# Kernel optimization log

Hardware: AMD Instinct MI355X
Metric: run time of the kernel (lower is better)

Reference implementation:

```python
import jax, jax.numpy as jnp
import numpy as np

B, S, H, L, NH, V = 8, 512, 768, 12, 12, 21128
DH = H // NH
FF = 4 * H
PAD_ID, SEP_ID = 0, 102
EPS = 1e-12


def _ln(x, g, b):
    mu = jnp.mean(x, axis=-1, keepdims=True)
    var = jnp.mean(jnp.square(x - mu), axis=-1, keepdims=True)
    return (x - mu) * jax.lax.rsqrt(var + EPS) * g + b


def setup_inputs() -> dict:
    key = jax.random.key(0)
    ks = jax.random.split(key, 24)
    # token ids with a per-sample [SEP] boundary and trailing padding
    ids = jax.random.randint(ks[0], (B, S), 1, V)
    qpos = jax.random.randint(ks[1], (B,), 16, 64)
    seqlen = jax.random.randint(ks[2], (B,), 384, S + 1)
    pos = jnp.arange(S)
    ids = jnp.where(pos[None, :] == qpos[:, None], SEP_ID, ids)
    ids = jnp.where(pos[None, :] < seqlen[:, None], ids, PAD_ID)

    w = lambda k, shape: (jax.random.normal(k, shape, dtype=jnp.float32) * 0.02)
    return {
        "input_ids": ids,
        "word_emb": w(ks[3], (V, H)),
        "pos_emb": w(ks[4], (S, H)),
        "type_emb": w(ks[5], (2, H)),
        "emb_ln_g": jnp.ones((H,), jnp.float32),
        "emb_ln_b": jnp.zeros((H,), jnp.float32),
        "attn_w": w(ks[6], (L, 4, H, H)),     # q,k,v,o projections
        "attn_b": w(ks[7], (L, 4, H)),
        "ln1_g": jnp.ones((L, H), jnp.float32),
        "ln1_b": jnp.zeros((L, H), jnp.float32),
        "ffn_w1": w(ks[8], (L, H, FF)),
        "ffn_b1": w(ks[9], (L, FF)),
        "ffn_w2": w(ks[10], (L, FF, H)),
        "ffn_b2": w(ks[11], (L, H)),
        "ln2_g": jnp.ones((L, H), jnp.float32),
        "ln2_b": jnp.zeros((L, H), jnp.float32),
        "cls_w": w(ks[12], (H, V)),
        "cls_b": jnp.zeros((V,), jnp.float32),
    }


def _qa_causal_bias(input_ids):
    # Faithful to make_qa_causal_mask: pad mask * (bidirectional over question,
    # causal over answer), boundary = first [SEP] position + 1 per sample.
    pad = input_ids != PAD_ID                                  # [B,S]
    qlen = jnp.argmax(input_ids == SEP_ID, axis=1) + 1          # [B]
    i = jnp.arange(S)[:, None]
    j = jnp.arange(S)[None, :]
    in_answer = (i[None] >= qlen[:, None, None]) & (j[None] >= qlen[:, None, None])
    causal_ok = jnp.where(in_answer, j <= i, True)              # [B,S,S]
    mask = pad[:, :, None] & pad[:, None, :] & causal_ok
    return jnp.where(mask, 0.0, -1e9).astype(jnp.float32)       # additive bias


def reference(input_ids, word_emb, pos_emb, type_emb, emb_ln_g, emb_ln_b,
              attn_w, attn_b, ln1_g, ln1_b, ffn_w1, ffn_b1, ffn_w2, ffn_b2,
              ln2_g, ln2_b, cls_w, cls_b):
    bias = _qa_causal_bias(input_ids)[:, None]                  # [B,1,S,S]
    h = word_emb[input_ids] + pos_emb[None, :S] + type_emb[0]
    h = _ln(h, emb_ln_g, emb_ln_b)
    scale = 1.0 / jnp.sqrt(jnp.float32(DH))
    for l in range(L):
        wq, wk, wv, wo = attn_w[l]
        bq, bk, bv, bo = attn_b[l]
        q = (h @ wq + bq).reshape(B, S, NH, DH)
        k = (h @ wk + bk).reshape(B, S, NH, DH)
        v = (h @ wv + bv).reshape(B, S, NH, DH)
        scores = jnp.einsum('bqhd,bkhd->bhqk', q, k) * scale + bias
        probs = jax.nn.softmax(scores, axis=-1)
        ctx = jnp.einsum('bhqk,bkhd->bqhd', probs, v).reshape(B, S, H)
        h = _ln(h + ctx @ wo + bo, ln1_g[l], ln1_b[l])
        ff = jax.nn.gelu(h @ ffn_w1[l] + ffn_b1[l], approximate=False) @ ffn_w2[l] + ffn_b2[l]
        h = _ln(h + ff, ln2_g[l], ln2_b[l])
    return h @ cls_w + cls_b                                    # [B,S,V] logits
```

## Files before the change

kernel.cpp:

```cpp
#include <hip/hip_runtime.h>
#include <hip/hip_bf16.h>
#include <stdint.h>

#define BB   8
#define SS   512
#define HH   768
#define LL   12
#define NHH  12
#define DHH  64
#define FFF  3072
#define VV   21128
#define PAD_ID 0
#define SEP_ID 102
#define BS   (BB*SS)
#define BSH  ((size_t)BS*HH)
#define BSFF ((size_t)BS*FFF)
#define QKVN (3*HH)

using bf16 = __hip_bfloat16;
typedef __attribute__((ext_vector_type(8))) short short8;
typedef __attribute__((ext_vector_type(4))) float f32x4;

__device__ __forceinline__ f32x4 Z4() { f32x4 z = {0.f, 0.f, 0.f, 0.f}; return z; }

__device__ __forceinline__ void gload16(void* lds, const void* g) {
    __builtin_amdgcn_global_load_lds(
        (const __attribute__((address_space(1))) uint32_t*)g,
        (__attribute__((address_space(3))) uint32_t*)(uint32_t)(uintptr_t)lds,
        16, 0, 0);
}

__device__ __forceinline__ void wait_vm0_barrier() {
    asm volatile("s_waitcnt vmcnt(0)" ::: "memory");
    __builtin_amdgcn_sched_barrier(0);
    __builtin_amdgcn_s_barrier();
    __builtin_amdgcn_sched_barrier(0);
}

__device__ __forceinline__ void wait_vm0_lgkm0_barrier() {
    asm volatile("s_waitcnt vmcnt(0) lgkmcnt(0)" ::: "memory");
    __builtin_amdgcn_sched_barrier(0);
    __builtin_amdgcn_s_barrier();
    __builtin_amdgcn_sched_barrier(0);
}

__global__ void __launch_bounds__(256) qlen_kernel(const int* __restrict__ ids,
                                                   int* __restrict__ qlen) {
    int b = blockIdx.x, tid = threadIdx.x;
    __shared__ int red[256];
    int best = 1 << 30;
    for (int j = tid; j < SS; j += 256)
        if (ids[b * SS + j] == SEP_ID) best = min(best, j);
    red[tid] = best; __syncthreads();
    for (int off = 128; off > 0; off >>= 1) {
        if (tid < off) red[tid] = min(red[tid], red[tid + off]);
        __syncthreads();
    }
    if (tid == 0) qlen[b] = (red[0] == (1 << 30) ? 0 : red[0]) + 1;
}

__device__ __forceinline__ float block_reduce_sum(float v, float* red, int tid) {
    red[tid] = v; __syncthreads();
    for (int off = 128; off > 0; off >>= 1) {
        if (tid < off) red[tid] += red[tid + off];
        __syncthreads();
    }
    float r = red[0]; __syncthreads();
    return r;
}

__global__ void __launch_bounds__(256) embed_ln_kernel(
    const int* __restrict__ ids, const float* __restrict__ we,
    const float* __restrict__ pe, const float* __restrict__ te,
    const float* __restrict__ g, const float* __restrict__ bt,
    float* __restrict__ h, bf16* __restrict__ hb) {
    int token = blockIdx.x, tid = threadIdx.x;
    int s = token % SS;
    int id = ids[token];
    __shared__ float red[256];
    float x[3];
#pragma unroll
    for (int i = 0; i < 3; ++i) {
        int idx = tid + i * 256;
        x[i] = we[(size_t)id * HH + idx] + pe[(size_t)s * HH + idx] + te[idx];
    }
    float sum = block_reduce_sum(x[0] + x[1] + x[2], red, tid);
    float mu = sum * (1.0f / HH);
    float vs = 0.f;
#pragma unroll
    for (int i = 0; i < 3; ++i) { float d = x[i] - mu; vs += d * d; }
    vs = block_reduce_sum(vs, red, tid);
    float rstd = rsqrtf(vs * (1.0f / HH) + 1e-12f);
    size_t base = (size_t)token * HH;
#pragma unroll
    for (int i = 0; i < 3; ++i) {
        int idx = tid + i * 256;
        float v = (x[i] - mu) * rstd * g[idx] + bt[idx];
        h[base + idx] = v;
        hb[base + idx] = __float2bfloat16(v);
    }
}

__global__ void __launch_bounds__(256) add_ln_kernel(
    float* __restrict__ h, const float* __restrict__ proj,
    const float* __restrict__ proj2,
    const float* __restrict__ g, const float* __restrict__ bt,
    bf16* __restrict__ hb) {
    int token = blockIdx.x, tid = threadIdx.x;
    __shared__ float red[256];
    size_t base = (size_t)token * HH;
    float x[3];
#pragma unroll
    for (int i = 0; i < 3; ++i) {
        int idx = tid + i * 256;
        x[i] = h[base + idx] + proj[base + idx] + proj2[base + idx];
    }
    float sum = block_reduce_sum(x[0] + x[1] + x[2], red, tid);
    float mu = sum * (1.0f / HH);
    float vs = 0.f;
#pragma unroll
    for (int i = 0; i < 3; ++i) { float d = x[i] - mu; vs += d * d; }
    vs = block_reduce_sum(vs, red, tid);
    float rstd = rsqrtf(vs * (1.0f / HH) + 1e-12f);
#pragma unroll
    for (int i = 0; i < 3; ++i) {
        int idx = tid + i * 256;
        float v = (x[i] - mu) * rstd * g[idx] + bt[idx];
        h[base + idx] = v;
        hb[base + idx] = __float2bfloat16(v);
    }
}

__global__ void __launch_bounds__(256) transp_conv(
    const float* __restrict__ in, bf16* __restrict__ out,
    int K, int N, size_t inStride, size_t outStride) {
    const float* src = in + (size_t)blockIdx.z * inStride;
    bf16* dst = out + (size_t)blockIdx.z * outStride;
    __shared__ float t[64][65];
    int n0 = blockIdx.x * 64, k0 = blockIdx.y * 64;
    int tid = threadIdx.x;
#pragma unroll
    for (int i = 0; i < 16; ++i) {
        int lin = tid + i * 256;
        int r = lin >> 6, c = lin & 63;
        int kk = k0 + r, nn = n0 + c;
        t[r][c] = (kk < K && nn < N) ? src[(size_t)kk * N + nn] : 0.f;
    }
    __syncthreads();
#pragma unroll
    for (int i = 0; i < 16; ++i) {
        int lin = tid + i * 256;
        int r = lin >> 6, c = lin & 63;
        int nn = n0 + r, kk = k0 + c;
        if (nn < N && kk < K)
            dst[(size_t)nn * K + kk] = __float2bfloat16(t[c][r]);
    }
}

__global__ void __launch_bounds__(256) vtrans_kernel(const bf16* __restrict__ v,
                                                     bf16* __restrict__ vT,
                                                     int ldv) {
    __shared__ bf16 t[64][66];
    int s0 = blockIdx.x * 64, h = blockIdx.y, b = blockIdx.z;
    int tid = threadIdx.x;
#pragma unroll
    for (int i = 0; i < 16; ++i) {
        int lin = tid + i * 256;
        int sr = lin >> 6, dc = lin & 63;
        t[sr][dc] = v[((size_t)(b * SS + s0 + sr)) * ldv + h * 64 + dc];
    }
    __syncthreads();
#pragma unroll
    for (int i = 0; i < 16; ++i) {
        int lin = tid + i * 256;
        int dr = lin >> 6, sc = lin & 63;
        vT[(((size_t)(b * NHH + h)) * 64 + dr) * SS + s0 + sc] = t[sc][dr];
    }
}

#define GBK 32

template <int TBM, int TBN, int OUT_BF16, int ACT>
__global__ void __launch_bounds__(256) gemm_bf16_kernel(
    const bf16* __restrict__ A, const bf16* __restrict__ BT,
    const float* __restrict__ bias, void* __restrict__ Cout,
    int M, int N, int K, int lda, int ldb, int ldc, size_t zStride) {
    constexpr int MFRAG = TBM / 32;
    constexpr int NFRAG = TBN / 32;
    constexpr int ABYTES = TBM * GBK * 2;
    constexpr int BBYTES = TBN * GBK * 2;
    __shared__ __align__(16) char As[2 * ABYTES];
    __shared__ __align__(16) char Bs[2 * BBYTES];
    int tid = threadIdx.x;
    int lane = tid & 63, wid = tid >> 6;

    int zz = blockIdx.z;
    const char* Ab = (const char*)(A + (size_t)zz * K);
    const char* Bb = (const char*)(BT + (size_t)zz * K);
    const float* biasz = (zz == 0) ? bias : nullptr;

    int nwg = gridDim.x * gridDim.y;
    int bid = blockIdx.y * gridDim.x + blockIdx.x;
    int swz = ((nwg & 7) == 0) ? ((bid & 7) * (nwg >> 3) + (bid >> 3)) : bid;
    int bx = swz % gridDim.x, by = swz / gridDim.x;
    int m0 = by * TBM, n0 = bx * TBN;
    int wr = (wid >> 1) * (TBM / 2), wc = (wid & 1) * (TBN / 2);

    f32x4 acc[MFRAG][NFRAG];
#pragma unroll
    for (int i = 0; i < MFRAG; ++i)
#pragma unroll
        for (int j = 0; j < NFRAG; ++j) acc[i][j] = Z4();

    auto stage = [&](int k0, int sel) {
#pragma unroll
        for (int i = 0; i < TBM / 64; ++i) {
            int lin = tid * 16 + i * 4096;
            int row = lin >> 6, slot = (lin >> 4) & 3;
            gload16(As + sel * ABYTES + lin,
                    Ab + ((size_t)(m0 + row) * lda + k0) * 2 +
                        ((slot ^ ((row >> 1) & 3)) << 4));
        }
#pragma unroll
        for (int i = 0; i < TBN / 64; ++i) {
            int lin = tid * 16 + i * 4096;
            int row = lin >> 6, slot = (lin >> 4) & 3;
            int nr = n0 + row; if (nr >= N) nr = N - 1;
            gload16(Bs + sel * BBYTES + lin,
                    Bb + ((size_t)nr * ldb + k0) * 2 +
                        ((slot ^ ((row >> 1) & 3)) << 4));
        }
    };

    const int T = K / GBK;
    stage(0, 0);
    wait_vm0_barrier();

    int cur = 0;
    for (int t = 0; t < T; ++t) {
        if (t + 1 < T) stage((t + 1) * GBK, cur ^ 1);

        const char* Ar = As + cur * ABYTES;
        const char* Br = Bs + cur * BBYTES;
        short8 af[MFRAG], bfr[NFRAG];
#pragma unroll
        for (int i = 0; i < MFRAG; ++i) {
            int ar = wr + i * 16 + (lane & 15);
            int slot = (lane >> 4) ^ ((ar >> 1) & 3);
            af[i] = *(const short8*)(Ar + ar * 64 + slot * 16);
        }
#pragma unroll
        for (int j = 0; j < NFRAG; ++j) {
            int br = wc + j * 16 + (lane & 15);
            int slot = (lane >> 4) ^ ((br >> 1) & 3);
            bfr[j] = *(const short8*)(Br + br * 64 + slot * 16);
        }
#pragma unroll
        for (int i = 0; i < MFRAG; ++i)
#pragma unroll
            for (int j = 0; j < NFRAG; ++j)
                acc[i][j] = __builtin_amdgcn_mfma_f32_16x16x32_bf16(
                    af[i], bfr[j], acc[i][j], 0, 0, 0);

        if (t + 1 < T) wait_vm0_barrier();
        cur ^= 1;
    }

    bool nfull = (n0 + TBN <= N);
#pragma unroll
    for (int i = 0; i < MFRAG; ++i) {
#pragma unroll
        for (int r = 0; r < 4; ++r) {
            int m = m0 + wr + i * 16 + (lane >> 4) * 4 + r;
#pragma unroll
            for (int j = 0; j < NFRAG; ++j) {
                int n = n0 + wc + j * 16 + (lane & 15);
                if (nfull || n < N) {
                    float v = acc[i][j][r] + (biasz ? biasz[n] : 0.f);
                    if (ACT) v = 0.5f * v * (1.0f + erff(v * 0.70710678118654752f));
                    if (OUT_BF16)
                        ((bf16*)Cout)[(size_t)m * ldc + n] = __float2bfloat16(v);
                    else
                        ((float*)Cout)[zz * zStride + (size_t)m * ldc + n] = v;
                }
            }
        }
    }
}

__global__ void __launch_bounds__(256) attn_mfma_kernel(
    const bf16* __restrict__ Q, const bf16* __restrict__ K,
    const bf16* __restrict__ VT, const int* __restrict__ ids,
    const int* __restrict__ qlen, bf16* __restrict__ att, int ld) {
    __shared__ __align__(16) bf16 Qs[64 * 64];
    __shared__ __align__(16) bf16 Ks[2][64 * 64];
    __shared__ __align__(16) bf16 Vs[2][64 * 64];
    __shared__ __align__(16) bf16 Ps[4 * 16 * 64];
    __shared__ float padj[2][64];

    int tid = threadIdx.x, lane = tid & 63, w = tid >> 6;
    int q0 = blockIdx.x * 64, h = blockIdx.y, b = blockIdx.z;
    int ql = qlen[b];

    const char* kbase0 = (const char*)K + ((size_t)(b * SS) * ld) * 2;
    const char* vbase0 = (const char*)VT + (((size_t)(b * NHH + h)) * 64) * SS * 2;

    auto stageKV = [&](int kv0, int sel) {
        int lin = tid * 16;
#pragma unroll
        for (int i = 0; i < 2; ++i, lin += 4096) {
            int row = lin >> 7, bir = lin & 127;
            int sbir = bir ^ ((row & 7) << 4);
            gload16((char*)Ks[sel] + lin,
                    kbase0 + (size_t)(kv0 + row) * (ld * 2) + h * 128 + sbir);
            gload16((char*)Vs[sel] + lin,
                    vbase0 + (size_t)row * (SS * 2) + (size_t)kv0 * 2 + sbir);
        }
        if (tid < 64)
            padj[sel][tid] = (ids[b * SS + kv0 + tid] != PAD_ID) ? 1.f : 0.f;
    };

    {
        const char* qbase =
            (const char*)Q + ((size_t)(b * SS + q0) * ld) * 2 + h * 128;
        int lin = tid * 16;
#pragma unroll
        for (int i = 0; i < 2; ++i, lin += 4096) {
            int row = lin >> 7, bir = lin & 127;
            int sbir = bir ^ ((row & 7) << 4);
            gload16((char*)Qs + lin, qbase + (size_t)row * (ld * 2) + sbir);
        }
    }
    stageKV(0, 0);
    int qrow_base = q0 + w * 16 + (lane >> 4) * 4;
    bool padq[4];
#pragma unroll
    for (int r = 0; r < 4; ++r)
        padq[r] = (ids[b * SS + qrow_base + r] != PAD_ID);

    wait_vm0_lgkm0_barrier();

    short8 aq[2];
#pragma unroll
    for (int ks = 0; ks < 2; ++ks) {
        int row = w * 16 + (lane & 15);
        int bir = ks * 64 + (lane >> 4) * 16;
        aq[ks] = *(const short8*)((const char*)Qs + row * 128 +
                                  (bir ^ ((row & 7) << 4)));
    }

    float m_run[4], l_run[4];
    f32x4 accO[4];
#pragma unroll
    for (int r = 0; r < 4; ++r) { m_run[r] = -1e30f; l_run[r] = 0.f; }
#pragma unroll
    for (int d = 0; d < 4; ++d) accO[d] = Z4();

    int cur = 0;
    for (int kv0 = 0; kv0 < SS; kv0 += 64) {
        if (kv0 + 64 < SS) stageKV(kv0 + 64, cur ^ 1);
        const char* kb = (const char*)Ks[cur];
        const char* vb = (const char*)Vs[cur];

        f32x4 accS[4];
        __builtin_amdgcn_s_setprio(1);
#pragma unroll
        for (int nf = 0; nf < 4; ++nf) {
            f32x4 z = Z4();
#pragma unroll
            for (int ks = 0; ks < 2; ++ks) {
                int row = nf * 16 + (lane & 15);
                int bir = ks * 64 + (lane >> 4) * 16;
                short8 bk = *(const short8*)(kb + row * 128 +
                                             (bir ^ ((row & 7) << 4)));
                z = __builtin_amdgcn_mfma_f32_16x16x32_bf16(aq[ks], bk, z, 0, 0, 0);
            }
            accS[nf] = z;
        }
        __builtin_amdgcn_s_setprio(0);

        float p[4][4];
#pragma unroll
        for (int r = 0; r < 4; ++r) {
            int qg = qrow_base + r;
            float mx = -1e30f;
#pragma unroll
            for (int nf = 0; nf < 4; ++nf) {
                int j = kv0 + nf * 16 + (lane & 15);
                bool ok = padq[r] && (padj[cur][nf * 16 + (lane & 15)] != 0.f) &&
                          ((qg < ql) || (j < ql) || (j <= qg));
                float s = accS[nf][r] * 0.125f + (ok ? 0.f : -1e9f);
                p[r][nf] = s;
                mx = fmaxf(mx, s);
            }
#pragma unroll
            for (int off = 1; off < 16; off <<= 1)
                mx = fmaxf(mx, __shfl_xor(mx, off));
            float mnew = fmaxf(m_run[r], mx);
            float fac = __expf(m_run[r] - mnew);
            m_run[r] = mnew;
            float rs = 0.f;
#pragma unroll
            for (int nf = 0; nf < 4; ++nf) {
                float e = __expf(p[r][nf] - mnew);
                p[r][nf] = e;
                rs += e;
            }
#pragma unroll
            for (int off = 1; off < 16; off <<= 1)
                rs += __shfl_xor(rs, off);
            l_run[r] = l_run[r] * fac + rs;
#pragma unroll
            for (int df = 0; df < 4; ++df) accO[df][r] *= fac;
        }

#pragma unroll
        for (int r = 0; r < 4; ++r) {
            int prow = (lane >> 4) * 4 + r;
#pragma unroll
            for (int nf = 0; nf < 4; ++nf) {
                int c = nf * 16 + (lane & 15);
                int byte = (c * 2) ^ ((prow & 7) << 4);
                *(bf16*)((char*)Ps + w * 2048 + prow * 128 + byte) =
                    __float2bfloat16(p[r][nf]);
            }
        }
        asm volatile("s_waitcnt lgkmcnt(0)" ::: "memory");
        __builtin_amdgcn_sched_barrier(0);

        __builtin_amdgcn_s_setprio(1);
#pragma unroll
        for (int ks = 0; ks < 2; ++ks) {
            int prow = lane & 15;
            int bir = ks * 64 + (lane >> 4) * 16;
            short8 ap = *(const short8*)((const char*)Ps + w * 2048 + prow * 128 +
                                         (bir ^ ((prow & 7) << 4)));
#pragma unroll
            for (int df = 0; df < 4; ++df) {
                int vrow = df * 16 + (lane & 15);
                short8 bv = *(const short8*)(vb + vrow * 128 +
                                             (bir ^ ((vrow & 7) << 4)));
                accO[df] = __builtin_amdgcn_mfma_f32_16x16x32_bf16(
                    ap, bv, accO[df], 0, 0, 0);
            }
        }
        __builtin_amdgcn_s_setprio(0);

        if (kv0 + 64 < SS) wait_vm0_lgkm0_barrier();
        cur ^= 1;
    }

#pragma unroll
    for (int r = 0; r < 4; ++r) {
        int qg = qrow_base + r;
        float inv = 1.0f / l_run[r];
#pragma unroll
        for (int df = 0; df < 4; ++df) {
            int d = df * 16 + (lane & 15);
            att[((size_t)(b * SS) + qg) * HH + h * 64 + d] =
                __float2bfloat16(accO[df][r] * inv);
        }
    }
}

extern "C" void kernel_launch(void* const* d_in, const int* in_sizes, int n_in,
                              void* d_out, int out_size, void* d_ws, size_t ws_size,
                              hipStream_t stream) {
    const int*   ids      = (const int*)d_in[0];
    const float* word_emb = (const float*)d_in[1];
    const float* pos_emb  = (const float*)d_in[2];
    const float* type_emb = (const float*)d_in[3];
    const float* emb_ln_g = (const float*)d_in[4];
    const float* emb_ln_b = (const float*)d_in[5];
    const float* attn_w   = (const float*)d_in[6];
    const float* attn_b   = (const float*)d_in[7];
    const float* ln1_g    = (const float*)d_in[8];
    const float* ln1_b    = (const float*)d_in[9];
    const float* ffn_w1   = (const float*)d_in[10];
    const float* ffn_b1   = (const float*)d_in[11];
    const float* ffn_w2   = (const float*)d_in[12];
    const float* ffn_b2   = (const float*)d_in[13];
    const float* ln2_g    = (const float*)d_in[14];
    const float* ln2_b    = (const float*)d_in[15];
    const float* cls_w    = (const float*)d_in[16];
    const float* cls_b    = (const float*)d_in[17];
    float* out = (float*)d_out;

    char* base = (char*)d_ws;
    size_t off = 0;
    auto take = [&](size_t bytes) {
        char* r = base + off;
        off += (bytes + 255) & ~(size_t)255;
        return r;
    };
    float* h    = (float*)take(BSH * 4);
    float* proj = (float*)take(2 * BSH * 4);
    bf16*  qkv  = (bf16*)take((size_t)BS * QKVN * 2);
    bf16*  vT   = (bf16*)take(BSH * 2);
    bf16*  attb = (bf16*)take(BSH * 2);
    bf16*  ffb  = (bf16*)take(BSFF * 2);
    bf16*  hb   = (bf16*)take(BSH * 2);
    int*   qlen = (int*)take(256);
    size_t commonEnd = off;

    const size_t szAttnW = (size_t)48 * HH * HH * 2;
    const size_t szW1    = (size_t)LL * HH * FFF * 2;
    const size_t szCls   = (size_t)VV * HH * 2;
    const size_t fullNeed = commonEnd + szAttnW + 2 * szW1 + szCls;
    bool fullMode = (ws_size >= fullNeed);

    bf16 *wAttnT = nullptr, *w1T = nullptr, *w2T = nullptr, *clsT = nullptr, *wrot = nullptr;
    if (fullMode) {
        wAttnT = (bf16*)take(szAttnW);
        w1T    = (bf16*)take(szW1);
        w2T    = (bf16*)take(szW1);
        clsT   = (bf16*)take(szCls);
    } else {
        wrot = (bf16*)take((size_t)HH * FFF * 2);
        clsT = (bf16*)proj;
    }

    auto convw = [&](const float* src, bf16* dst, int K, int N) {
        dim3 g((N + 63) / 64, (K + 63) / 64, 1);
        transp_conv<<<g, 256, 0, stream>>>(src, dst, K, N, (size_t)0, (size_t)0);
    };

    qlen_kernel<<<BB, 256, 0, stream>>>(ids, qlen);

    if (fullMode) {
        transp_conv<<<dim3(12, 12, 48), 256, 0, stream>>>(
            attn_w, wAttnT, HH, HH, (size_t)HH * HH, (size_t)HH * HH);
        transp_conv<<<dim3(FFF / 64, HH / 64, LL), 256, 0, stream>>>(
            ffn_w1, w1T, HH, FFF, (size_t)HH * FFF, (size_t)HH * FFF);
        transp_conv<<<dim3(HH / 64, FFF / 64, LL), 256, 0, stream>>>(
            ffn_w2, w2T, FFF, HH, (size_t)HH * FFF, (size_t)HH * FFF);
        transp_conv<<<dim3((VV + 63) / 64, HH / 64, 1), 256, 0, stream>>>(
            cls_w, clsT, HH, VV, (size_t)0, (size_t)0);
    }

    embed_ln_kernel<<<BS, 256, 0, stream>>>(ids, word_emb, pos_emb, type_emb,
                                            emb_ln_g, emb_ln_b, h, hb);

    dim3 gQKV(QKVN / 128, BS / 128, 1);
    dim3 gWo(HH / 64, BS / 128, 2);
    dim3 gFF1(FFF / 128, BS / 128, 1);
    dim3 gFF2(HH / 64, BS / 128, 2);
    dim3 gCls((VV + 127) / 128, BS / 128, 1);
    dim3 gAttn(SS / 64, NHH, BB);
    dim3 gVT(SS / 64, NHH, BB);

    for (int l = 0; l < LL; ++l) {
        const float* wq32 = attn_w + (size_t)l * 4 * HH * HH;
        const float* wo32 = wq32 + (size_t)3 * HH * HH;
        const float* bqkv = attn_b + (size_t)l * 4 * HH;
        const float* bo   = bqkv + 3 * HH;

        bf16 *wqkvT, *woT, *w1Tl, *w2Tl;
        if (fullMode) {
            wqkvT = wAttnT + (size_t)(l * 4) * HH * HH;
            woT   = wAttnT + (size_t)(l * 4 + 3) * HH * HH;
            w1Tl  = w1T + (size_t)l * HH * FFF;
            w2Tl  = w2T + (size_t)l * HH * FFF;
        } else {
            wqkvT = woT = w1Tl = w2Tl = wrot;
        }

        if (!fullMode) {
            convw(wq32, wrot, HH, HH);
            convw(wq32 + (size_t)HH * HH, wrot + (size_t)HH * HH, HH, HH);
            convw(wq32 + (size_t)2 * HH * HH, wrot + (size_t)2 * HH * HH, HH, HH);
        }
        gemm_bf16_kernel<128, 128, 1, 0><<<gQKV, 256, 0, stream>>>(
            hb, wqkvT, bqkv, qkv, BS, QKVN, HH, HH, HH, QKVN, 0);

        vtrans_kernel<<<gVT, 256, 0, stream>>>(qkv + 2 * HH, vT, QKVN);
        attn_mfma_kernel<<<gAttn, 256, 0, stream>>>(
            qkv, qkv + HH, vT, ids, qlen, attb, QKVN);

        if (!fullMode) convw(wo32, wrot, HH, HH);
        gemm_bf16_kernel<128, 64, 0, 0><<<gWo, 256, 0, stream>>>(
            attb, woT, bo, proj, BS, HH, HH / 2, HH, HH, HH, BSH);
        add_ln_kernel<<<BS, 256, 0, stream>>>(h, proj, proj + BSH,
                                              ln1_g + (size_t)l * HH,
                                              ln1_b + (size_t)l * HH, hb);

        if (!fullMode) convw(ffn_w1 + (size_t)l * HH * FFF, wrot, HH, FFF);
        gemm_bf16_kernel<128, 128, 1, 1><<<gFF1, 256, 0, stream>>>(
            hb, w1Tl, ffn_b1 + (size_t)l * FFF, ffb, BS, FFF, HH, HH, HH, FFF, 0);
        if (!fullMode) convw(ffn_w2 + (size_t)l * HH * FFF, wrot, FFF, HH);
        gemm_bf16_kernel<128, 64, 0, 0><<<gFF2, 256, 0, stream>>>(
            ffb, w2Tl, ffn_b2 + (size_t)l * HH, proj, BS, HH, FFF / 2, FFF, FFF,
            HH, BSH);
        add_ln_kernel<<<BS, 256, 0, stream>>>(h, proj, proj + BSH,
                                              ln2_g + (size_t)l * HH,
                                              ln2_b + (size_t)l * HH, hb);
    }

    if (!fullMode) convw(cls_w, clsT, HH, VV);
    gemm_bf16_kernel<128, 128, 0, 0><<<gCls, 256, 0, stream>>>(
        hb, clsT, cls_b, out, BS, VV, HH, HH, HH, VV, 0);
}
```

Baseline: 2.787 ms.

## Triple-buffer GEMM K-loop, group-swizzle tiles, and double query rows per attention block

The GEMM kernel moves from double to triple buffering in LDS and issues loads two K-steps ahead. It waits with partial vmcnt so only the oldest stage must land before each barrier, which aims to hide global-load latency. The tile mapping is regrouped into 8-row M groups to improve L2 reuse of A and B tiles. The attention kernel now processes 128 query rows per block, 32 per wave, so each K/V tile staged in LDS serves twice as many queries. The cost is more LDS and registers, lower occupancy, and half as many attention blocks.

```diff
diff --git a/kernel.cpp b/kernel.cpp
--- a/kernel.cpp
+++ b/kernel.cpp
@@ -30,9 +30,18 @@
         16, 0, 0);
 }
 
-__device__ __forceinline__ void wait_vm0_barrier() {
-    asm volatile("s_waitcnt vmcnt(0)" ::: "memory");
+template <int N>
+__device__ __forceinline__ void waitvm() {
+    if constexpr (N == 0) asm volatile("s_waitcnt vmcnt(0)" ::: "memory");
+    else if constexpr (N == 2) asm volatile("s_waitcnt vmcnt(2)" ::: "memory");
+    else if constexpr (N == 3) asm volatile("s_waitcnt vmcnt(3)" ::: "memory");
+    else if constexpr (N == 4) asm volatile("s_waitcnt vmcnt(4)" ::: "memory");
+    else if constexpr (N == 6) asm volatile("s_waitcnt vmcnt(6)" ::: "memory");
+    else asm volatile("s_waitcnt vmcnt(8)" ::: "memory");
     __builtin_amdgcn_sched_barrier(0);
+}
+
+__device__ __forceinline__ void barrier_raw() {
     __builtin_amdgcn_s_barrier();
     __builtin_amdgcn_sched_barrier(0);
 }
@@ -189,8 +198,9 @@
     constexpr int NFRAG = TBN / 32;
     constexpr int ABYTES = TBM * GBK * 2;
     constexpr int BBYTES = TBN * GBK * 2;
-    __shared__ __align__(16) char As[2 * ABYTES];
-    __shared__ __align__(16) char Bs[2 * BBYTES];
+    constexpr int LPS = TBM / 64 + TBN / 64;
+    __shared__ __align__(16) char As[3 * ABYTES];
+    __shared__ __align__(16) char Bs[3 * BBYTES];
     int tid = threadIdx.x;
     int lane = tid & 63, wid = tid >> 6;
 
@@ -199,10 +209,16 @@
     const char* Bb = (const char*)(BT + (size_t)zz * K);
     const float* biasz = (zz == 0) ? bias : nullptr;
 
-    int nwg = gridDim.x * gridDim.y;
-    int bid = blockIdx.y * gridDim.x + blockIdx.x;
+    int gN = gridDim.x, gM = gridDim.y;
+    int nwg = gN * gM;
+    int bid = blockIdx.y * gN + blockIdx.x;
     int swz = ((nwg & 7) == 0) ? ((bid & 7) * (nwg >> 3) + (bid >> 3)) : bid;
-    int bx = swz % gridDim.x, by = swz / gridDim.x;
+    int width = 8 * gN;
+    int grp = swz / width, rem = swz % width;
+    int gh = min(8, gM - grp * 8);
+    int by = grp * 8 + rem % gh;
+    int bx = rem / gh;
+
     int m0 = by * TBM, n0 = bx * TBN;
     int wr = (wid >> 1) * (TBM / 2), wc = (wid & 1) * (TBN / 2);
 
@@ -234,14 +250,15 @@
 
     const int T = K / GBK;
     stage(0, 0);
-    wait_vm0_barrier();
-
-    int cur = 0;
+    stage(GBK, 1);
+    waitvm<LPS>();
+    barrier_raw();
+
     for (int t = 0; t < T; ++t) {
-        if (t + 1 < T) stage((t + 1) * GBK, cur ^ 1);
-
-        const char* Ar = As + cur * ABYTES;
-        const char* Br = Bs + cur * BBYTES;
+        if (t + 2 < T) stage((t + 2) * GBK, (t + 2) % 3);
+
+        const char* Ar = As + (t % 3) * ABYTES;
+        const char* Br = Bs + (t % 3) * BBYTES;
         short8 af[MFRAG], bfr[NFRAG];
 #pragma unroll
         for (int i = 0; i < MFRAG; ++i) {
@@ -262,8 +279,11 @@
                 acc[i][j] = __builtin_amdgcn_mfma_f32_16x16x32_bf16(
                     af[i], bfr[j], acc[i][j], 0, 0, 0);
 
-        if (t + 1 < T) wait_vm0_barrier();
-        cur ^= 1;
+        if (t + 1 < T) {
+            if (t + 2 < T) waitvm<LPS>();
+            else           waitvm<0>();
+            barrier_raw();
+        }
     }
 
     bool nfull = (n0 + TBN <= N);
@@ -292,14 +312,14 @@
     const bf16* __restrict__ Q, const bf16* __restrict__ K,
     const bf16* __restrict__ VT, const int* __restrict__ ids,
     const int* __restrict__ qlen, bf16* __restrict__ att, int ld) {
-    __shared__ __align__(16) bf16 Qs[64 * 64];
+    __shared__ __align__(16) bf16 Qs[128 * 64];
     __shared__ __align__(16) bf16 Ks[2][64 * 64];
     __shared__ __align__(16) bf16 Vs[2][64 * 64];
-    __shared__ __align__(16) bf16 Ps[4 * 16 * 64];
+    __shared__ __align__(16) bf16 Ps[4 * 32 * 64];
     __shared__ float padj[2][64];
 
     int tid = threadIdx.x, lane = tid & 63, w = tid >> 6;
-    int q0 = blockIdx.x * 64, h = blockIdx.y, b = blockIdx.z;
+    int q0 = blockIdx.x * 128, h = blockIdx.y, b = blockIdx.z;
     int ql = qlen[b];
 
     const char* kbase0 = (const char*)K + ((size_t)(b * SS) * ld) * 2;
@@ -323,38 +343,49 @@
     {
         const char* qbase =
             (const char*)Q + ((size_t)(b * SS + q0) * ld) * 2 + h * 128;
-        int lin = tid * 16;
-#pragma unroll
-        for (int i = 0; i < 2; ++i, lin += 4096) {
+#pragma unroll
+        for (int i = 0; i < 4; ++i) {
+            int lin = tid * 16 + i * 4096;
             int row = lin >> 7, bir = lin & 127;
             int sbir = bir ^ ((row & 7) << 4);
             gload16((char*)Qs + lin, qbase + (size_t)row * (ld * 2) + sbir);
         }
     }
     stageKV(0, 0);
-    int qrow_base = q0 + w * 16 + (lane >> 4) * 4;
-    bool padq[4];
-#pragma unroll
-    for (int r = 0; r < 4; ++r)
-        padq[r] = (ids[b * SS + qrow_base + r] != PAD_ID);
+
+    int qrb[2];
+    bool padq[2][4];
+#pragma unroll
+    for (int rf = 0; rf < 2; ++rf) {
+        qrb[rf] = q0 + w * 32 + rf * 16 + (lane >> 4) * 4;
+#pragma unroll
+        for (int r = 0; r < 4; ++r)
+            padq[rf][r] = (ids[b * SS + qrb[rf] + r] != PAD_ID);
+    }
 
     wait_vm0_lgkm0_barrier();
 
-    short8 aq[2];
-#pragma unroll
-    for (int ks = 0; ks < 2; ++ks) {
-        int row = w * 16 + (lane & 15);
-        int bir = ks * 64 + (lane >> 4) * 16;
-        aq[ks] = *(const short8*)((const char*)Qs + row * 128 +
-                                  (bir ^ ((row & 7) << 4)));
-    }
-
-    float m_run[4], l_run[4];
-    f32x4 accO[4];
-#pragma unroll
-    for (int r = 0; r < 4; ++r) { m_run[r] = -1e30f; l_run[r] = 0.f; }
-#pragma unroll
-    for (int d = 0; d < 4; ++d) accO[d] = Z4();
+    short8 aq[2][2];
+#pragma unroll
+    for (int rf = 0; rf < 2; ++rf)
+#pragma unroll
+        for (int ks = 0; ks < 2; ++ks) {
+            int row = w * 32 + rf * 16 + (lane & 15);
+            int bir = ks * 64 + (lane >> 4) * 16;
+            aq[rf][ks] = *(const short8*)((const char*)Qs + row * 128 +
+                                          (bir ^ ((row & 7) << 4)));
+        }
+
+    float m_run[2][4], l_run[2][4];
+    f32x4 accO[2][4];
+#pragma unroll
+    for (int rf = 0; rf < 2; ++rf)
+#pragma unroll
+        for (int r = 0; r < 4; ++r) { m_run[rf][r] = -1e30f; l_run[rf][r] = 0.f; }
+#pragma unroll
+    for (int rf = 0; rf < 2; ++rf)
+#pragma unroll
+        for (int d = 0; d < 4; ++d) accO[rf][d] = Z4();
 
     int cur = 0;
     for (int kv0 = 0; kv0 < SS; kv0 += 64) {
@@ -362,67 +393,72 @@
         const char* kb = (const char*)Ks[cur];
         const char* vb = (const char*)Vs[cur];
 
-        f32x4 accS[4];
-        __builtin_amdgcn_s_setprio(1);
-#pragma unroll
-        for (int nf = 0; nf < 4; ++nf) {
-            f32x4 z = Z4();
-#pragma unroll
-            for (int ks = 0; ks < 2; ++ks) {
-                int row = nf * 16 + (lane & 15);
-                int bir = ks * 64 + (lane >> 4) * 16;
-                short8 bk = *(const short8*)(kb + row * 128 +
-                                             (bir ^ ((row & 7) << 4)));
-                z = __builtin_amdgcn_mfma_f32_16x16x32_bf16(aq[ks], bk, z, 0, 0, 0);
+#pragma unroll
+        for (int rf = 0; rf < 2; ++rf) {
+            f32x4 accS[4];
+            __builtin_amdgcn_s_setprio(1);
+#pragma unroll
+            for (int nf = 0; nf < 4; ++nf) {
+                f32x4 z = Z4();
+#pragma unroll
+                for (int ks = 0; ks < 2; ++ks) {
+                    int row = nf * 16 + (lane & 15);
+                    int bir = ks * 64 + (lane >> 4) * 16;
+                    short8 bk = *(const short8*)(kb + row * 128 +
+                                                 (bir ^ ((row & 7) << 4)));
+                    z = __builtin_amdgcn_mfma_f32_16x16x32_bf16(aq[rf][ks], bk, z,
+                                                                0, 0, 0);
+                }
+                accS[nf] = z;
             }
-            accS[nf] = z;
-        }
-        __builtin_amdgcn_s_setprio(0);
-
-        float p[4][4];
-#pragma unroll
-        for (int r = 0; r < 4; ++r) {
-            int qg = qrow_base + r;
-            float mx = -1e30f;
-#pragma unroll
-            for (int nf = 0; nf < 4; ++nf) {
-                int j = kv0 + nf * 16 + (lane & 15);
-                bool ok = padq[r] && (padj[cur][nf * 16 + (lane & 15)] != 0.f) &&
-                          ((qg < ql) || (j < ql) || (j <= qg));
-                float s = accS[nf][r] * 0.125f + (ok ? 0.f : -1e9f);
-                p[r][nf] = s;
-                mx = fmaxf(mx, s);
+            __builtin_amdgcn_s_setprio(0);
+
+            float p[4][4];
+#pragma unroll
+            for (int r = 0; r < 4; ++r) {
+                int qg = qrb[rf] + r;
+                float mx = -1e30f;
+#pragma unroll
+                for (int nf = 0; nf < 4; ++nf) {
+                    int j = kv0 + nf * 16 + (lane & 15);
+                    bool ok = padq[rf][r] &&
+                              (padj[cur][nf * 16 + (lane & 15)] != 0.f) &&
+                              ((qg < ql) || (j < ql) || (j <= qg));
+                    float s = accS[nf][r] * 0.125f + (ok ? 0.f : -1e9f);
+                    p[r][nf] = s;
+                    mx = fmaxf(mx, s);
+                }
+#pragma unroll
+                for (int off = 1; off < 16; off <<= 1)
+                    mx = fmaxf(mx, __shfl_xor(mx, off));
+                float mnew = fmaxf(m_run[rf][r], mx);
+                float fac = __expf(m_run[rf][r] - mnew);
+                m_run[rf][r] = mnew;
+                float rs = 0.f;
+#pragma unroll
+                for (int nf = 0; nf < 4; ++nf) {
+                    float e = __expf(p[r][nf] - mnew);
+                    p[r][nf] = e;
+                    rs += e;
+                }
+#pragma unroll
+                for (int off = 1; off < 16; off <<= 1)
+                    rs += __shfl_xor(rs, off);
+                l_run[rf][r] = l_run[rf][r] * fac + rs;
+#pragma unroll
+                for (int df = 0; df < 4; ++df) accO[rf][df][r] *= fac;
             }
-#pragma unroll
-            for (int off = 1; off < 16; off <<= 1)
-                mx = fmaxf(mx, __shfl_xor(mx, off));
-            float mnew = fmaxf(m_run[r], mx);
-            float fac = __expf(m_run[r] - mnew);
-            m_run[r] = mnew;
-            float rs = 0.f;
-#pragma unroll
-            for (int nf = 0; nf < 4; ++nf) {
-                float e = __expf(p[r][nf] - mnew);
-                p[r][nf] = e;
-                rs += e;
-            }
-#pragma unroll
-            for (int off = 1; off < 16; off <<= 1)
-                rs += __shfl_xor(rs, off);
-            l_run[r] = l_run[r] * fac + rs;
-#pragma unroll
-            for (int df = 0; df < 4; ++df) accO[df][r] *= fac;
-        }
-
-#pragma unroll
-        for (int r = 0; r < 4; ++r) {
-            int prow = (lane >> 4) * 4 + r;
-#pragma unroll
-            for (int nf = 0; nf < 4; ++nf) {
-                int c = nf * 16 + (lane & 15);
-                int byte = (c * 2) ^ ((prow & 7) << 4);
-                *(bf16*)((char*)Ps + w * 2048 + prow * 128 + byte) =
-                    __float2bfloat16(p[r][nf]);
+
+#pragma unroll
+            for (int r = 0; r < 4; ++r) {
+                int prow = rf * 16 + (lane >> 4) * 4 + r;
+#pragma unroll
+                for (int nf = 0; nf < 4; ++nf) {
+                    int c = nf * 16 + (lane & 15);
+                    int byte = (c * 2) ^ ((prow & 7) << 4);
+                    *(bf16*)((char*)Ps + w * 4096 + prow * 128 + byte) =
+                        __float2bfloat16(p[r][nf]);
+                }
             }
         }
         asm volatile("s_waitcnt lgkmcnt(0)" ::: "memory");
@@ -431,17 +467,24 @@
         __builtin_amdgcn_s_setprio(1);
 #pragma unroll
         for (int ks = 0; ks < 2; ++ks) {
-            int prow = lane & 15;
-            int bir = ks * 64 + (lane >> 4) * 16;
-            short8 ap = *(const short8*)((const char*)Ps + w * 2048 + prow * 128 +
-                                         (bir ^ ((prow & 7) << 4)));
+            short8 ap[2];
+#pragma unroll
+            for (int rf = 0; rf < 2; ++rf) {
+                int prow = rf * 16 + (lane & 15);
+                int bir = ks * 64 + (lane >> 4) * 16;
+                ap[rf] = *(const short8*)((const char*)Ps + w * 4096 + prow * 128 +
+                                          (bir ^ ((prow & 7) << 4)));
+            }
 #pragma unroll
             for (int df = 0; df < 4; ++df) {
                 int vrow = df * 16 + (lane & 15);
+                int bir = ks * 64 + (lane >> 4) * 16;
                 short8 bv = *(const short8*)(vb + vrow * 128 +
                                              (bir ^ ((vrow & 7) << 4)));
-                accO[df] = __builtin_amdgcn_mfma_f32_16x16x32_bf16(
-                    ap, bv, accO[df], 0, 0, 0);
+#pragma unroll
+                for (int rf = 0; rf < 2; ++rf)
+                    accO[rf][df] = __builtin_amdgcn_mfma_f32_16x16x32_bf16(
+                        ap[rf], bv, accO[rf][df], 0, 0, 0);
             }
         }
         __builtin_amdgcn_s_setprio(0);
@@ -451,16 +494,18 @@
     }
 
 #pragma unroll
-    for (int r = 0; r < 4; ++r) {
-        int qg = qrow_base + r;
-        float inv = 1.0f / l_run[r];
-#pragma unroll
-        for (int df = 0; df < 4; ++df) {
-            int d = df * 16 + (lane & 15);
-            att[((size_t)(b * SS) + qg) * HH + h * 64 + d] =
-                __float2bfloat16(accO[df][r] * inv);
-        }
-    }
+    for (int rf = 0; rf < 2; ++rf)
+#pragma unroll
+        for (int r = 0; r < 4; ++r) {
+            int qg = qrb[rf] + r;
+            float inv = 1.0f / l_run[rf][r];
+#pragma unroll
+            for (int df = 0; df < 4; ++df) {
+                int d = df * 16 + (lane & 15);
+                att[((size_t)(b * SS) + qg) * HH + h * 64 + d] =
+                    __float2bfloat16(accO[rf][df][r] * inv);
+            }
+        }
 }
 
 extern "C" void kernel_launch(void* const* d_in, const int* in_sizes, int n_in,
@@ -546,7 +591,7 @@
     dim3 gFF1(FFF / 128, BS / 128, 1);
     dim3 gFF2(HH / 64, BS / 128, 2);
     dim3 gCls((VV + 127) / 128, BS / 128, 1);
-    dim3 gAttn(SS / 64, NHH, BB);
+    dim3 gAttn(SS / 128, NHH, BB);
     dim3 gVT(SS / 64, NHH, BB);
 
     for (int l = 0; l < LL; ++l) {
```

New measurement: 3.020 ms. 1.08x slower.

## Triple-buffer GEMM loads with partial vmcnt waits and grouped tile order

Applied to the files above, without the earlier changes.

The bf16 GEMM moves from double to triple buffering in LDS. It prefetches two K-steps ahead and waits with a partial vmcnt, so one stage of global loads stays in flight across each barrier. K, the leading dimensions and N become template constants, so index math and bounds checks are resolved at compile time. The block order is regrouped into 8-row bands to improve L2 reuse. The cost is more LDS per block, which may reduce occupancy.

```diff
diff --git a/kernel.cpp b/kernel.cpp
--- a/kernel.cpp
+++ b/kernel.cpp
@@ -30,9 +30,18 @@
         16, 0, 0);
 }
 
-__device__ __forceinline__ void wait_vm0_barrier() {
-    asm volatile("s_waitcnt vmcnt(0)" ::: "memory");
+template <int N>
+__device__ __forceinline__ void waitvm() {
+    if constexpr (N == 0) asm volatile("s_waitcnt vmcnt(0)" ::: "memory");
+    else if constexpr (N == 2) asm volatile("s_waitcnt vmcnt(2)" ::: "memory");
+    else if constexpr (N == 3) asm volatile("s_waitcnt vmcnt(3)" ::: "memory");
+    else if constexpr (N == 4) asm volatile("s_waitcnt vmcnt(4)" ::: "memory");
+    else if constexpr (N == 6) asm volatile("s_waitcnt vmcnt(6)" ::: "memory");
+    else asm volatile("s_waitcnt vmcnt(8)" ::: "memory");
     __builtin_amdgcn_sched_barrier(0);
+}
+
+__device__ __forceinline__ void barrier_raw() {
     __builtin_amdgcn_s_barrier();
     __builtin_amdgcn_sched_barrier(0);
 }
@@ -180,29 +189,35 @@
 
 #define GBK 32
 
-template <int TBM, int TBN, int OUT_BF16, int ACT>
+template <int TBM, int TBN, int OUT_BF16, int ACT, int KK, int LDA, int LDB,
+          int LDC, int NN>
 __global__ void __launch_bounds__(256) gemm_bf16_kernel(
     const bf16* __restrict__ A, const bf16* __restrict__ BT,
-    const float* __restrict__ bias, void* __restrict__ Cout,
-    int M, int N, int K, int lda, int ldb, int ldc, size_t zStride) {
+    const float* __restrict__ bias, void* __restrict__ Cout, size_t zStride) {
     constexpr int MFRAG = TBM / 32;
     constexpr int NFRAG = TBN / 32;
     constexpr int ABYTES = TBM * GBK * 2;
     constexpr int BBYTES = TBN * GBK * 2;
-    __shared__ __align__(16) char As[2 * ABYTES];
-    __shared__ __align__(16) char Bs[2 * BBYTES];
+    constexpr int LPS = TBM / 64 + TBN / 64;
+    __shared__ __align__(16) char As[3 * ABYTES];
+    __shared__ __align__(16) char Bs[3 * BBYTES];
     int tid = threadIdx.x;
     int lane = tid & 63, wid = tid >> 6;
 
     int zz = blockIdx.z;
-    const char* Ab = (const char*)(A + (size_t)zz * K);
-    const char* Bb = (const char*)(BT + (size_t)zz * K);
-    const float* biasz = (zz == 0) ? bias : nullptr;
-
-    int nwg = gridDim.x * gridDim.y;
-    int bid = blockIdx.y * gridDim.x + blockIdx.x;
+    const char* Ab = (const char*)(A + (size_t)zz * KK);
+    const char* Bb = (const char*)(BT + (size_t)zz * KK);
+
+    int gN = gridDim.x, gM = gridDim.y;
+    int nwg = gN * gM;
+    int bid = blockIdx.y * gN + blockIdx.x;
     int swz = ((nwg & 7) == 0) ? ((bid & 7) * (nwg >> 3) + (bid >> 3)) : bid;
-    int bx = swz % gridDim.x, by = swz / gridDim.x;
+    int width = 8 * gN;
+    int grp = swz / width, rem = swz % width;
+    int gh = min(8, gM - grp * 8);
+    int by = grp * 8 + rem % gh;
+    int bx = rem / gh;
+
     int m0 = by * TBM, n0 = bx * TBN;
     int wr = (wid >> 1) * (TBM / 2), wc = (wid & 1) * (TBN / 2);
 
@@ -218,30 +233,32 @@
             int lin = tid * 16 + i * 4096;
             int row = lin >> 6, slot = (lin >> 4) & 3;
             gload16(As + sel * ABYTES + lin,
-                    Ab + ((size_t)(m0 + row) * lda + k0) * 2 +
+                    Ab + ((size_t)(m0 + row) * LDA + k0) * 2 +
                         ((slot ^ ((row >> 1) & 3)) << 4));
         }
 #pragma unroll
         for (int i = 0; i < TBN / 64; ++i) {
             int lin = tid * 16 + i * 4096;
             int row = lin >> 6, slot = (lin >> 4) & 3;
-            int nr = n0 + row; if (nr >= N) nr = N - 1;
+            int nr = n0 + row;
+            if constexpr (NN % TBN != 0) { if (nr >= NN) nr = NN - 1; }
             gload16(Bs + sel * BBYTES + lin,
-                    Bb + ((size_t)nr * ldb + k0) * 2 +
+                    Bb + ((size_t)nr * LDB + k0) * 2 +
                         ((slot ^ ((row >> 1) & 3)) << 4));
         }
     };
 
-    const int T = K / GBK;
+    constexpr int T = KK / GBK;
     stage(0, 0);
-    wait_vm0_barrier();
-
-    int cur = 0;
+    stage(GBK, 1);
+    waitvm<LPS>();
+    barrier_raw();
+
     for (int t = 0; t < T; ++t) {
-        if (t + 1 < T) stage((t + 1) * GBK, cur ^ 1);
-
-        const char* Ar = As + cur * ABYTES;
-        const char* Br = Bs + cur * BBYTES;
+        if (t + 2 < T) stage((t + 2) * GBK, (t + 2) % 3);
+
+        const char* Ar = As + (t % 3) * ABYTES;
+        const char* Br = Bs + (t % 3) * BBYTES;
         short8 af[MFRAG], bfr[NFRAG];
 #pragma unroll
         for (int i = 0; i < MFRAG; ++i) {
@@ -262,11 +279,14 @@
                 acc[i][j] = __builtin_amdgcn_mfma_f32_16x16x32_bf16(
                     af[i], bfr[j], acc[i][j], 0, 0, 0);
 
-        if (t + 1 < T) wait_vm0_barrier();
-        cur ^= 1;
-    }
-
-    bool nfull = (n0 + TBN <= N);
+        if (t + 1 < T) {
+            if (t + 2 < T) waitvm<LPS>();
+            else           waitvm<0>();
+            barrier_raw();
+        }
+    }
+
+    bool nfull = (NN % TBN == 0) || (n0 + TBN <= NN);
 #pragma unroll
     for (int i = 0; i < MFRAG; ++i) {
 #pragma unroll
@@ -275,13 +295,13 @@
 #pragma unroll
             for (int j = 0; j < NFRAG; ++j) {
                 int n = n0 + wc + j * 16 + (lane & 15);
-                if (nfull || n < N) {
-                    float v = acc[i][j][r] + (biasz ? biasz[n] : 0.f);
+                if (nfull || n < NN) {
+                    float v = acc[i][j][r] + ((zz == 0) ? bias[n] : 0.f);
                     if (ACT) v = 0.5f * v * (1.0f + erff(v * 0.70710678118654752f));
                     if (OUT_BF16)
-                        ((bf16*)Cout)[(size_t)m * ldc + n] = __float2bfloat16(v);
+                        ((bf16*)Cout)[(size_t)m * LDC + n] = __float2bfloat16(v);
                     else
-                        ((float*)Cout)[zz * zStride + (size_t)m * ldc + n] = v;
+                        ((float*)Cout)[zz * zStride + (size_t)m * LDC + n] = v;
                 }
             }
         }
@@ -570,33 +590,33 @@
             convw(wq32 + (size_t)HH * HH, wrot + (size_t)HH * HH, HH, HH);
             convw(wq32 + (size_t)2 * HH * HH, wrot + (size_t)2 * HH * HH, HH, HH);
         }
-        gemm_bf16_kernel<128, 128, 1, 0><<<gQKV, 256, 0, stream>>>(
-            hb, wqkvT, bqkv, qkv, BS, QKVN, HH, HH, HH, QKVN, 0);
+        gemm_bf16_kernel<128, 128, 1, 0, HH, HH, HH, QKVN, QKVN>
+            <<<gQKV, 256, 0, stream>>>(hb, wqkvT, bqkv, qkv, 0);
 
         vtrans_kernel<<<gVT, 256, 0, stream>>>(qkv + 2 * HH, vT, QKVN);
         attn_mfma_kernel<<<gAttn, 256, 0, stream>>>(
             qkv, qkv + HH, vT, ids, qlen, attb, QKVN);
 
         if (!fullMode) convw(wo32, wrot, HH, HH);
-        gemm_bf16_kernel<128, 64, 0, 0><<<gWo, 256, 0, stream>>>(
-            attb, woT, bo, proj, BS, HH, HH / 2, HH, HH, HH, BSH);
+        gemm_bf16_kernel<128, 64, 0, 0, HH / 2, HH, HH, HH, HH>
+            <<<gWo, 256, 0, stream>>>(attb, woT, bo, proj, BSH);
         add_ln_kernel<<<BS, 256, 0, stream>>>(h, proj, proj + BSH,
                                               ln1_g + (size_t)l * HH,
                                               ln1_b + (size_t)l * HH, hb);
 
         if (!fullMode) convw(ffn_w1 + (size_t)l * HH * FFF, wrot, HH, FFF);
-        gemm_bf16_kernel<128, 128, 1, 1><<<gFF1, 256, 0, stream>>>(
-            hb, w1Tl, ffn_b1 + (size_t)l * FFF, ffb, BS, FFF, HH, HH, HH, FFF, 0);
+        gemm_bf16_kernel<128, 128, 1, 1, HH, HH, HH, FFF, FFF>
+            <<<gFF1, 256, 0, stream>>>(hb, w1Tl, ffn_b1 + (size_t)l * FFF, ffb, 0);
         if (!fullMode) convw(ffn_w2 + (size_t)l * HH * FFF, wrot, FFF, HH);
-        gemm_bf16_kernel<128, 64, 0, 0><<<gFF2, 256, 0, stream>>>(
-            ffb, w2Tl, ffn_b2 + (size_t)l * HH, proj, BS, HH, FFF / 2, FFF, FFF,
-            HH, BSH);
+        gemm_bf16_kernel<128, 64, 0, 0, FFF / 2, FFF, FFF, HH, HH>
+            <<<gFF2, 256, 0, stream>>>(ffb, w2Tl, ffn_b2 + (size_t)l * HH, proj,
+                                       BSH);
         add_ln_kernel<<<BS, 256, 0, stream>>>(h, proj, proj + BSH,
                                               ln2_g + (size_t)l * HH,
                                               ln2_b + (size_t)l * HH, hb);
     }
 
     if (!fullMode) convw(cls_w, clsT, HH, VV);
-    gemm_bf16_kernel<128, 128, 0, 0><<<gCls, 256, 0, stream>>>(
-        hb, clsT, cls_b, out, BS, VV, HH, HH, HH, VV, 0);
-}
+    gemm_bf16_kernel<128, 128, 0, 0, HH, HH, HH, VV, VV>
+        <<<gCls, 256, 0, stream>>>(hb, clsT, cls_b, out, 0);
+}
```

Measured after the change: 2.828 ms. About the same (+1.5%).
